# Optimization experiments

Hardware: AMD Instinct MI355X
Metric: run time of the kernel (lower is better)

## Reference

```python
import jax, jax.numpy as jnp
import numpy as np

NORM_EPS = 1e-6   # config.norm_eps
MAG_EPS = 1e-6    # config.magnitude_eps


def setup_inputs() -> dict:
    key = jax.random.key(0)
    k0, k1, k2, k3, k4, k5 = jax.random.split(key, 6)
    B, S, IN, OUT, R, L = 4, 2048, 2048, 2048, 4, 16
    x = jax.random.normal(k0, (B, S, IN), dtype=jnp.float32)
    # frozen quantization indices (buffer _indices), values in [0, lut_size)
    indices = jax.random.randint(k1, (OUT, IN), 0, L, dtype=jnp.int32)
    # monotonic LUT in [-1, 1] (make_lut with include_zero=False)
    lut = jnp.linspace(-1.0, 1.0, L, dtype=jnp.float32)
    scale_A = jax.random.normal(k2, (OUT, R), dtype=jnp.float32)
    scale_B = jax.random.normal(k3, (R, IN), dtype=jnp.float32)
    rank_magnitude = jax.random.uniform(k4, (R,), dtype=jnp.float32)
    bias = jax.random.normal(k5, (OUT,), dtype=jnp.float32) * 0.01
    return {"x": x, "indices": indices, "lut": lut, "scale_A": scale_A,
            "scale_B": scale_B, "rank_magnitude": rank_magnitude, "bias": bias}


def reference(x, indices, lut, scale_A, scale_B, rank_magnitude, bias):
    # _get_normalized_scales: force_positive_scales='abs', magnitude_activation='softplus'
    A = jnp.abs(scale_A)                                            # [out, r]
    A_dir = A / jnp.maximum(jnp.linalg.norm(A, axis=0, keepdims=True), NORM_EPS)
    Bm = jnp.abs(scale_B)                                           # [r, in]
    B_dir = Bm / jnp.maximum(jnp.linalg.norm(Bm, axis=1, keepdims=True), NORM_EPS)
    g = jax.nn.softplus(rank_magnitude) + MAG_EPS                   # [r]
    # LUT dequant: Q = lut[_indices], [out, in]
    Q = lut[indices]
    # rank-by-rank forward: y = sum_k g_k * (a_k \odot (Q (b_k \odot x))) + bias
    # t[b,s,r,o] = sum_i x[b,s,i] * B_dir[r,i] * Q[o,i]
    t = jnp.einsum('bsi,ri,oi->bsro', x, B_dir, Q)
    y = jnp.einsum('bsro,or,r->bso', t, A_dir, g) + bias
    return y
```

## Files before the change

### kernel.cpp

```cpp
#include <hip/hip_runtime.h>

#define IN_DIM  2048
#define OUT_DIM 2048
#define MROWS   8192
#define RANK    4

typedef unsigned short ushort_t;
typedef __attribute__((ext_vector_type(8))) short  short8;
typedef __attribute__((ext_vector_type(4))) float  floatx4;

__device__ __forceinline__ unsigned short f2bf(float f) {
  union { float f; unsigned int u; } v; v.f = f;
  unsigned int r = v.u + 0x7fffu + ((v.u >> 16) & 1u);
  return (unsigned short)(r >> 16);
}

__device__ __forceinline__ void gload16(const ushort_t* g, short* l) {
  __builtin_amdgcn_global_load_lds(
      (const __attribute__((address_space(1))) void*)g,
      (__attribute__((address_space(3))) void*)l, 16, 0, 0);
}

__global__ void coef_kernel(const float* __restrict__ sA, const float* __restrict__ sB,
                            const float* __restrict__ mag, float* __restrict__ cOut) {
  __shared__ float part[8][256];
  __shared__ float tot[8];
  int t = threadIdx.x;
  float sa[4] = {0.f, 0.f, 0.f, 0.f};
  for (int o = t; o < OUT_DIM; o += 256) {
    float4 v = *(const float4*)(sA + o * 4);
    sa[0] += v.x * v.x; sa[1] += v.y * v.y; sa[2] += v.z * v.z; sa[3] += v.w * v.w;
  }
  float sb[4] = {0.f, 0.f, 0.f, 0.f};
  for (int r = 0; r < 4; ++r)
    for (int i = t; i < IN_DIM; i += 256) { float v = sB[r * IN_DIM + i]; sb[r] += v * v; }
  for (int q = 0; q < 4; ++q) { part[q][t] = sa[q]; part[4 + q][t] = sb[q]; }
  __syncthreads();
  if (t < 8) { float s = 0.f; for (int j = 0; j < 256; ++j) s += part[t][j]; tot[t] = s; }
  __syncthreads();
  if (t < 4) {
    float g  = log1pf(expf(mag[t])) + 1e-6f;
    float na = fmaxf(sqrtf(tot[t]),     1e-6f);
    float nb = fmaxf(sqrtf(tot[4 + t]), 1e-6f);
    cOut[t] = g / (na * nb);
  }
}

__global__ void prep_kernel(const float* __restrict__ x, ushort_t* __restrict__ xb,
                            const int* __restrict__ idx, const float* __restrict__ lut,
                            const float* __restrict__ sA, const float* __restrict__ sB,
                            const float* __restrict__ c, ushort_t* __restrict__ W) {
  int t = threadIdx.x;
  if (blockIdx.x < 8192) {
    size_t i = ((size_t)blockIdx.x * 256 + t) * 8;
    float4 a = *(const float4*)(x + i);
    float4 b = *(const float4*)(x + i + 4);
    uint4 o4;
    o4.x = (unsigned)f2bf(a.x) | ((unsigned)f2bf(a.y) << 16);
    o4.y = (unsigned)f2bf(a.z) | ((unsigned)f2bf(a.w) << 16);
    o4.z = (unsigned)f2bf(b.x) | ((unsigned)f2bf(b.y) << 16);
    o4.w = (unsigned)f2bf(b.z) | ((unsigned)f2bf(b.w) << 16);
    *(uint4*)(xb + i) = o4;
  } else {
    __shared__ float aA[4];
    __shared__ float lutS[16];
    int o = blockIdx.x - 8192;
    if (t < 4)  aA[t]   = fabsf(sA[o * 4 + t]) * c[t];
    if (t < 16) lutS[t] = lut[t];
    __syncthreads();
    int i = t * 8;
    const int4* ip4 = (const int4*)(idx + (size_t)o * IN_DIM + i);
    int4 i0 = ip4[0], i1 = ip4[1];
    int ii[8] = {i0.x, i0.y, i0.z, i0.w, i1.x, i1.y, i1.z, i1.w};
    unsigned short u[8];
    #pragma unroll
    for (int j = 0; j < 8; ++j) {
      float s = aA[0] * fabsf(sB[0 * IN_DIM + i + j])
              + aA[1] * fabsf(sB[1 * IN_DIM + i + j])
              + aA[2] * fabsf(sB[2 * IN_DIM + i + j])
              + aA[3] * fabsf(sB[3 * IN_DIM + i + j]);
      u[j] = f2bf(lutS[ii[j]] * s);
    }
    uint4 o4;
    o4.x = (unsigned)u[0] | ((unsigned)u[1] << 16);
    o4.y = (unsigned)u[2] | ((unsigned)u[3] << 16);
    o4.z = (unsigned)u[4] | ((unsigned)u[5] << 16);
    o4.w = (unsigned)u[6] | ((unsigned)u[7] << 16);
    *(uint4*)(W + (size_t)o * IN_DIM + i) = o4;
  }
}

__global__ __launch_bounds__(256) void gemm_kernel(const ushort_t* __restrict__ A,
                                                   const ushort_t* __restrict__ W,
                                                   const float* __restrict__ bias,
                                                   float* __restrict__ C) {
  __shared__ short As[128 * 32];
  __shared__ short Bs[128 * 32];
  const int t    = threadIdx.x;
  const int lane = t & 63;
  const int wid  = t >> 6;
  const int wr   = wid >> 1;
  const int wc   = wid & 1;
  const int rowBase = blockIdx.y * 128;
  const int colBase = blockIdx.x * 128;

  floatx4 acc[4][4];
  #pragma unroll
  for (int i = 0; i < 4; ++i)
    #pragma unroll
    for (int j = 0; j < 4; ++j) acc[i][j] = (floatx4){0.f, 0.f, 0.f, 0.f};

  const int row0 = t >> 2;
  const int c0   = t & 3;
  const int kc0  = c0 ^ ((row0 >> 1) & 3);
  const ushort_t* a0 = A + (size_t)(rowBase + row0) * IN_DIM + kc0 * 8;
  const ushort_t* a1 = A + (size_t)(rowBase + row0 + 64) * IN_DIM + kc0 * 8;
  const ushort_t* b0 = W + (size_t)(colBase + row0) * IN_DIM + kc0 * 8;
  const ushort_t* b1 = W + (size_t)(colBase + row0 + 64) * IN_DIM + kc0 * 8;
  short* lA0 = As + (wid * 64) * 8;
  short* lA1 = As + (256 + wid * 64) * 8;
  short* lB0 = Bs + (wid * 64) * 8;
  short* lB1 = Bs + (256 + wid * 64) * 8;

  const int rA   = lane & 15;
  const int slot = ((rA >> 1) & 3) ^ (lane >> 4);
  const int kOff = slot * 8;

  for (int k0 = 0; k0 < IN_DIM; k0 += 32) {
    gload16(a0 + k0, lA0);
    gload16(a1 + k0, lA1);
    gload16(b0 + k0, lB0);
    gload16(b1 + k0, lB1);
    __syncthreads();

    short8 af[4], bf[4];
    #pragma unroll
    for (int mi = 0; mi < 4; ++mi)
      af[mi] = *(const short8*)(As + (wr * 64 + mi * 16 + rA) * 32 + kOff);
    #pragma unroll
    for (int ni = 0; ni < 4; ++ni)
      bf[ni] = *(const short8*)(Bs + (wc * 64 + ni * 16 + rA) * 32 + kOff);
    #pragma unroll
    for (int mi = 0; mi < 4; ++mi)
      #pragma unroll
      for (int ni = 0; ni < 4; ++ni)
        acc[mi][ni] = __builtin_amdgcn_mfma_f32_16x16x32_bf16(af[mi], bf[ni], acc[mi][ni], 0, 0, 0);
    __syncthreads();
  }

  const int mB = rowBase + wr * 64 + (lane >> 4) * 4;
  const int nB = colBase + wc * 64 + (lane & 15);
  #pragma unroll
  for (int ni = 0; ni < 4; ++ni) {
    float bv = bias[nB + ni * 16];
    #pragma unroll
    for (int mi = 0; mi < 4; ++mi)
      #pragma unroll
      for (int r = 0; r < 4; ++r)
        C[(size_t)(mB + mi * 16 + r) * OUT_DIM + (nB + ni * 16)] = acc[mi][ni][r] + bv;
  }
}

extern "C" void kernel_launch(void* const* d_in, const int* in_sizes, int n_in,
                              void* d_out, int out_size, void* d_ws, size_t ws_size,
                              hipStream_t stream) {
  const float* x    = (const float*)d_in[0];
  const int*   idx  = (const int*)d_in[1];
  const float* lut  = (const float*)d_in[2];
  const float* sA   = (const float*)d_in[3];
  const float* sB   = (const float*)d_in[4];
  const float* mag  = (const float*)d_in[5];
  const float* bias = (const float*)d_in[6];
  float* y = (float*)d_out;

  char* ws = (char*)d_ws;
  float*    c  = (float*)ws;
  ushort_t* W  = (ushort_t*)(ws + 256);
  ushort_t* xb = (ushort_t*)(ws + 256 + (size_t)OUT_DIM * IN_DIM * 2);

  coef_kernel<<<1, 256, 0, stream>>>(sA, sB, mag, c);
  prep_kernel<<<8192 + OUT_DIM, 256, 0, stream>>>(x, xb, idx, lut, sA, sB, c, W);
  dim3 g(OUT_DIM / 128, MROWS / 128);
  gemm_kernel<<<g, 256, 0, stream>>>(xb, W, bias, y);
}
```

Before: 245.3 us.

## Rewrite GEMM as 256x256 tile, 8-wave, double-buffered pipelined kernel

Replaces the 128x128 single-buffered GEMM with a 256x256 tile using 512 threads, BK=64, and two LDS buffers. Global-to-LDS loads for the next tiles are interleaved across four MFMA phases, gated by explicit vmcnt waits and raw barriers, with s_setprio raised around the MFMA bursts. The aim is to overlap memory loads with matrix math and to raise arithmetic intensity per tile. The cost is 128KB of LDS per block and heavy accumulator register use, which may limit occupancy, and the hand-written waitcnt schedule is fragile.

```diff
diff --git a/kernel.cpp b/kernel.cpp
--- a/kernel.cpp
+++ b/kernel.cpp
@@ -4,6 +4,7 @@
 #define OUT_DIM 2048
 #define MROWS   8192
 #define RANK    4
+#define BK      64
 
 typedef unsigned short ushort_t;
 typedef __attribute__((ext_vector_type(8))) short  short8;
@@ -90,71 +91,134 @@
   }
 }
 
-__global__ __launch_bounds__(256) void gemm_kernel(const ushort_t* __restrict__ A,
-                                                   const ushort_t* __restrict__ W,
-                                                   const float* __restrict__ bias,
-                                                   float* __restrict__ C) {
-  __shared__ short As[128 * 32];
-  __shared__ short Bs[128 * 32];
+
+#define MFMA16(a, b, c) __builtin_amdgcn_mfma_f32_16x16x32_bf16(a, b, c, 0, 0, 0)
+
+__device__ __forceinline__ void barrier_raw() {
+  asm volatile("" ::: "memory");
+  __builtin_amdgcn_s_barrier();
+  asm volatile("" ::: "memory");
+}
+
+__device__ __forceinline__ void stage_half(const ushort_t* gbase, short* ldsbase,
+                                           int tile, int h, int wid) {
+  gload16(gbase + (size_t)h * 64 * IN_DIM + (size_t)tile * BK,
+          ldsbase + (h * 512 + wid * 64) * 8);
+  gload16(gbase + ((size_t)h * 64 + 128) * IN_DIM + (size_t)tile * BK,
+          ldsbase + (1024 + h * 512 + wid * 64) * 8);
+}
+
+template <int MQ, bool FIRST, typename StageFn>
+__device__ __forceinline__ void phase(const short* aRd, const short* bRd,
+                                      int ko0, int ko1,
+                                      floatx4 (&acc)[8][4],
+                                      short8 (&bf0)[4], short8 (&bf1)[4],
+                                      StageFn&& stage, int vm) {
+  if (FIRST) {
+    #pragma unroll
+    for (int ni = 0; ni < 4; ++ni) {
+      bf0[ni] = *(const short8*)(bRd + ni * 1024 + ko0);
+      bf1[ni] = *(const short8*)(bRd + ni * 1024 + ko1);
+    }
+  }
+  short8 a0k0 = *(const short8*)(aRd + (2 * MQ) * 1024 + ko0);
+  short8 a0k1 = *(const short8*)(aRd + (2 * MQ) * 1024 + ko1);
+  short8 a1k0 = *(const short8*)(aRd + (2 * MQ + 1) * 1024 + ko0);
+  short8 a1k1 = *(const short8*)(aRd + (2 * MQ + 1) * 1024 + ko1);
+  stage();
+  if (vm == 6)      asm volatile("s_waitcnt vmcnt(6)" ::: "memory");
+  else if (vm == 0) asm volatile("s_waitcnt vmcnt(0)" ::: "memory");
+  barrier_raw();
+  __builtin_amdgcn_s_setprio(1);
+  #pragma unroll
+  for (int ni = 0; ni < 4; ++ni) {
+    acc[2 * MQ    ][ni] = MFMA16(a0k0, bf0[ni], acc[2 * MQ    ][ni]);
+    acc[2 * MQ    ][ni] = MFMA16(a0k1, bf1[ni], acc[2 * MQ    ][ni]);
+    acc[2 * MQ + 1][ni] = MFMA16(a1k0, bf0[ni], acc[2 * MQ + 1][ni]);
+    acc[2 * MQ + 1][ni] = MFMA16(a1k1, bf1[ni], acc[2 * MQ + 1][ni]);
+  }
+  __builtin_amdgcn_s_setprio(0);
+  barrier_raw();
+}
+
+__global__ __launch_bounds__(512, 2) void gemm_kernel(const ushort_t* __restrict__ A,
+                                                      const ushort_t* __restrict__ W,
+                                                      const float* __restrict__ bias,
+                                                      float* __restrict__ C) {
+  __shared__ short lA0[16384];
+  __shared__ short lB0[16384];
+  __shared__ short lA1[16384];
+  __shared__ short lB1[16384];
+
   const int t    = threadIdx.x;
   const int lane = t & 63;
   const int wid  = t >> 6;
-  const int wr   = wid >> 1;
-  const int wc   = wid & 1;
-  const int rowBase = blockIdx.y * 128;
-  const int colBase = blockIdx.x * 128;
-
-  floatx4 acc[4][4];
+  const int wr   = wid >> 2;
+  const int wc   = wid & 3;
+  const int rowBase = blockIdx.y * 256;
+  const int colBase = blockIdx.x * 256;
+
+  const int srcRow   = wid * 8 + (lane >> 3);
+  const int srcChunk = (lane & 7) ^ (lane >> 3);
+  const ushort_t* gA = A + (size_t)(rowBase + srcRow) * IN_DIM + srcChunk * 8;
+  const ushort_t* gB = W + (size_t)(colBase + srcRow) * IN_DIM + srcChunk * 8;
+
+  const int rA  = lane & 15;
+  const int kh  = lane >> 4;
+  const int sw  = rA & 7;
+  const int ko0 = ((kh)     ^ sw) * 8;
+  const int ko1 = ((4 + kh) ^ sw) * 8;
+  const short* aRd0 = lA0 + (wr * 128 + rA) * 64;
+  const short* bRd0 = lB0 + (wc * 64  + rA) * 64;
+  const short* aRd1 = lA1 + (wr * 128 + rA) * 64;
+  const short* bRd1 = lB1 + (wc * 64  + rA) * 64;
+
+  floatx4 acc[8][4];
   #pragma unroll
-  for (int i = 0; i < 4; ++i)
+  for (int i = 0; i < 8; ++i)
     #pragma unroll
     for (int j = 0; j < 4; ++j) acc[i][j] = (floatx4){0.f, 0.f, 0.f, 0.f};
-
-  const int row0 = t >> 2;
-  const int c0   = t & 3;
-  const int kc0  = c0 ^ ((row0 >> 1) & 3);
-  const ushort_t* a0 = A + (size_t)(rowBase + row0) * IN_DIM + kc0 * 8;
-  const ushort_t* a1 = A + (size_t)(rowBase + row0 + 64) * IN_DIM + kc0 * 8;
-  const ushort_t* b0 = W + (size_t)(colBase + row0) * IN_DIM + kc0 * 8;
-  const ushort_t* b1 = W + (size_t)(colBase + row0 + 64) * IN_DIM + kc0 * 8;
-  short* lA0 = As + (wid * 64) * 8;
-  short* lA1 = As + (256 + wid * 64) * 8;
-  short* lB0 = Bs + (wid * 64) * 8;
-  short* lB1 = Bs + (256 + wid * 64) * 8;
-
-  const int rA   = lane & 15;
-  const int slot = ((rA >> 1) & 3) ^ (lane >> 4);
-  const int kOff = slot * 8;
-
-  for (int k0 = 0; k0 < IN_DIM; k0 += 32) {
-    gload16(a0 + k0, lA0);
-    gload16(a1 + k0, lA1);
-    gload16(b0 + k0, lB0);
-    gload16(b1 + k0, lB1);
-    __syncthreads();
-
-    short8 af[4], bf[4];
-    #pragma unroll
-    for (int mi = 0; mi < 4; ++mi)
-      af[mi] = *(const short8*)(As + (wr * 64 + mi * 16 + rA) * 32 + kOff);
-    #pragma unroll
-    for (int ni = 0; ni < 4; ++ni)
-      bf[ni] = *(const short8*)(Bs + (wc * 64 + ni * 16 + rA) * 32 + kOff);
-    #pragma unroll
-    for (int mi = 0; mi < 4; ++mi)
-      #pragma unroll
-      for (int ni = 0; ni < 4; ++ni)
-        acc[mi][ni] = __builtin_amdgcn_mfma_f32_16x16x32_bf16(af[mi], bf[ni], acc[mi][ni], 0, 0, 0);
-    __syncthreads();
-  }
-
-  const int mB = rowBase + wr * 64 + (lane >> 4) * 4;
+  short8 bf0[4], bf1[4];
+
+  stage_half(gA, lA0, 0, 0, wid);
+  stage_half(gA, lA0, 0, 1, wid);
+  stage_half(gB, lB0, 0, 0, wid);
+  stage_half(gB, lB0, 0, 1, wid);
+  stage_half(gB, lB1, 1, 0, wid);
+  stage_half(gB, lB1, 1, 1, wid);
+  stage_half(gA, lA1, 1, 0, wid);
+  asm volatile("s_waitcnt vmcnt(6)" ::: "memory");
+  barrier_raw();
+
+  #pragma unroll 1
+  for (int i = 0; i < 16; ++i) {
+    const int  t2   = 2 * i + 2, t3 = 2 * i + 3;
+    const bool more = (i < 15);
+    phase<0, true >(aRd0, bRd0, ko0, ko1, acc, bf0, bf1,
+                    [&] { stage_half(gA, lA1, 2 * i + 1, 1, wid); }, -1);
+    phase<1, false>(aRd0, bRd0, ko0, ko1, acc, bf0, bf1,
+                    [&] { if (more) stage_half(gB, lB0, t2, 0, wid); }, -1);
+    phase<2, false>(aRd0, bRd0, ko0, ko1, acc, bf0, bf1,
+                    [&] { if (more) stage_half(gB, lB0, t2, 1, wid); }, -1);
+    phase<3, false>(aRd0, bRd0, ko0, ko1, acc, bf0, bf1,
+                    [&] { if (more) stage_half(gA, lA0, t2, 0, wid); }, more ? 6 : 0);
+    phase<0, true >(aRd1, bRd1, ko0, ko1, acc, bf0, bf1,
+                    [&] { if (more) stage_half(gA, lA0, t2, 1, wid); }, -1);
+    phase<1, false>(aRd1, bRd1, ko0, ko1, acc, bf0, bf1,
+                    [&] { if (more) stage_half(gB, lB1, t3, 0, wid); }, -1);
+    phase<2, false>(aRd1, bRd1, ko0, ko1, acc, bf0, bf1,
+                    [&] { if (more) stage_half(gB, lB1, t3, 1, wid); }, -1);
+    phase<3, false>(aRd1, bRd1, ko0, ko1, acc, bf0, bf1,
+                    [&] { if (more) stage_half(gA, lA1, t3, 0, wid); }, more ? 6 : -1);
+  }
+
+  const int mB = rowBase + wr * 128 + (lane >> 4) * 4;
   const int nB = colBase + wc * 64 + (lane & 15);
   #pragma unroll
   for (int ni = 0; ni < 4; ++ni) {
     float bv = bias[nB + ni * 16];
     #pragma unroll
-    for (int mi = 0; mi < 4; ++mi)
+    for (int mi = 0; mi < 8; ++mi)
       #pragma unroll
       for (int r = 0; r < 4; ++r)
         C[(size_t)(mB + mi * 16 + r) * OUT_DIM + (nB + ni * 16)] = acc[mi][ni][r] + bv;
@@ -180,6 +244,6 @@
 
   coef_kernel<<<1, 256, 0, stream>>>(sA, sB, mag, c);
   prep_kernel<<<8192 + OUT_DIM, 256, 0, stream>>>(x, xb, idx, lut, sA, sB, c, W);
-  dim3 g(OUT_DIM / 128, MROWS / 128);
-  gemm_kernel<<<g, 256, 0, stream>>>(xb, W, bias, y);
-}
+  dim3 g(OUT_DIM / 256, MROWS / 256);
+  gemm_kernel<<<g, 512, 0, stream>>>(xb, W, bias, y);
+}
```

Result: faster. 224.4 us (-8.5%).
